# Performance work log

Measured on AMD Instinct MI355X. Metric: run time of the kernel, lower is better.

Reference implementation:

```python
import jax, jax.numpy as jnp
import numpy as np

B, N = 8, 2048          # clouds x points per cloud
M1, M2 = 1024, 256      # centroids after ratio 0.5, then 0.25
K = 64                  # max_num_neighbors
R1, R2 = 0.2, 0.4       # radii
CURV_K = 10             # knn for curvature
CURV_SCALAR = 10.0      # Net(curvature_scalar)
NEG = -1e30


def _sqdist(a, b):
    # squared pairwise distances [len(a), len(b)] without an [.,.,3] intermediate
    return jnp.sum(a * a, -1)[:, None] + jnp.sum(b * b, -1)[None, :] - 2.0 * (a @ b.T)


def _mlp3(x, Wa, ba, Wb, bb, Wc, bc):
    # torch_geometric MLP: Linear+ReLU hidden layers, plain last layer
    h = jax.nn.relu(x @ Wa + ba)
    h = jax.nn.relu(h @ Wb + bb)
    return h @ Wc + bc


def _curvature(pos):
    # per-point surface variation lambda_min / sum(lambda) over k-NN covariance
    d2 = _sqdist(pos, pos)                        # [N,N]
    _, idx = jax.lax.top_k(-d2, CURV_K)           # k nearest (incl. self)
    nbr = pos[idx]                                # [N,k,3]
    c = nbr - jnp.mean(nbr, 1, keepdims=True)
    cov = jnp.einsum('nki,nkj->nij', c, c) / CURV_K
    ev = jnp.linalg.eigvalsh(cov)                 # ascending
    return ev[:, 0] / (jnp.sum(ev, -1) + 1e-8)


def _fps_weighted(pos, curv, m):
    # farthest point sampling, min-distance score weighted by curvature
    w = 1.0 + CURV_SCALAR * curv
    d0 = jnp.sum((pos - pos[0]) ** 2, -1)
    def step(min_d2, _):
        i = jnp.argmax(min_d2 * w)
        nd = jnp.sum((pos - pos[i]) ** 2, -1)
        return jnp.minimum(min_d2, nd), i
    _, rest = jax.lax.scan(step, d0, None, length=m - 1)
    return jnp.concatenate([jnp.zeros((1,), rest.dtype), rest])


def _sa(x, pos, curv, m, r, params):
    # SAModule: weighted FPS -> radius grouping (cap K) -> PointNetConv (gather, MLP, max)
    idx = _fps_weighted(pos, curv, m)
    cpos = pos[idx]                               # [m,3]
    d2 = _sqdist(cpos, pos)                       # [m,N]
    score = jnp.where(d2 <= r * r, -d2, NEG)
    vals, nidx = jax.lax.top_k(score, K)          # up to K nearest within radius
    mask = vals > NEG * 0.5                       # [m,K]
    rel = pos[nidx] - cpos[:, None, :]            # [m,K,3]
    feats = rel if x is None else jnp.concatenate([x[nidx], rel], -1)
    msg = _mlp3(feats, *params)                   # [m,K,F]
    msg = jnp.where(mask[:, :, None], msg, NEG)
    out = jnp.max(msg, 1)                         # scatter-max aggregation
    out = jnp.where(jnp.any(mask, 1)[:, None], out, 0.0)  # empty groups -> 0
    return out, cpos, curv[idx]


def _forward(pos, W1a, b1a, W1b, b1b, W1c, b1c, W2a, b2a, W2b, b2b, W2c, b2c,
             W3a, b3a, W3b, b3b, W3c, b3c, Wh1, bh1, Wh2, bh2, Wh3, bh3):
    p1 = (W1a, b1a, W1b, b1b, W1c, b1c)
    p2 = (W2a, b2a, W2b, b2b, W2c, b2c)
    p3 = (W3a, b3a, W3b, b3b, W3c, b3c)
    def cloud(p):
        curv = _curvature(p)
        x1, pos1, c1 = _sa(None, p, curv, M1, R1, p1)
        x2, pos2, _ = _sa(x1, pos1, c1, M2, R2, p2)
        g = _mlp3(jnp.concatenate([x2, pos2], -1), *p3)   # [M2,1024]
        return jnp.max(g, 0)                              # global max pool
    gfeat = jax.vmap(cloud)(pos.reshape(B, N, 3))          # [B,1024]
    logits = _mlp3(gfeat, Wh1, bh1, Wh2, bh2, Wh3, bh3)    # dropout (eval) = id
    return jax.nn.log_softmax(logits, -1)


_LAYERS = [("W1a", "b1a", 3, 64), ("W1b", "b1b", 64, 64), ("W1c", "b1c", 64, 128),
           ("W2a", "b2a", 131, 128), ("W2b", "b2b", 128, 128), ("W2c", "b2c", 128, 256),
           ("W3a", "b3a", 259, 256), ("W3b", "b3b", 256, 512), ("W3c", "b3c", 512, 1024),
           ("Wh1", "bh1", 1024, 512), ("Wh2", "bh2", 512, 256), ("Wh3", "bh3", 256, 10)]


def setup_inputs() -> dict:
    key = jax.random.key(0)
    ks = iter(jax.random.split(key, 2 * len(_LAYERS) + 1))
    inp = {"pos": jax.random.uniform(next(ks), (B * N, 3), jnp.float32)}
    for wn, bn, fi, fo in _LAYERS:
        inp[wn] = jax.random.normal(next(ks), (fi, fo), jnp.float32) / np.sqrt(fi)
        inp[bn] = jnp.zeros((fo,), jnp.float32)
    return inp


def reference(pos, W1a, b1a, W1b, b1b, W1c, b1c, W2a, b2a, W2b, b2b, W2c, b2c,
              W3a, b3a, W3b, b3b, W3c, b3c, Wh1, bh1, Wh2, bh2, Wh3, bh3):
    return _forward(pos, W1a, b1a, W1b, b1b, W1c, b1c, W2a, b2a, W2b, b2b, W2c, b2c,
                    W3a, b3a, W3b, b3b, W3c, b3c, Wh1, bh1, Wh2, bh2, Wh3, bh3)
```

## Files before the change

### kernel.cpp

```cpp
#include <hip/hip_runtime.h>
#include <hip/hip_fp16.h>
#include <math.h>

#define TID threadIdx.x

typedef _Float16 h2vec __attribute__((ext_vector_type(2)));
typedef _Float16 f16x8 __attribute__((ext_vector_type(8)));
typedef float f32x4 __attribute__((ext_vector_type(4)));
typedef float f32x2v __attribute__((ext_vector_type(2)));

#if __has_builtin(__builtin_elementwise_fma)
#define EFMA(a, b, c) __builtin_elementwise_fma((a), (b), (c))
#else
static __device__ __forceinline__ f32x2v EFMA(f32x2v a, f32x2v b, f32x2v c) {
    f32x2v r;
    r.x = fmaf(a.x, b.x, c.x);
    r.y = fmaf(a.y, b.y, c.y);
    return r;
}
#endif

static __device__ __forceinline__ float fdot2(unsigned a, unsigned b, float c) {
    h2vec av, bv;
    __builtin_memcpy(&av, &a, 4);
    __builtin_memcpy(&bv, &b, 4);
    return __builtin_amdgcn_fdot2(av, bv, c, false);
}

static __device__ __forceinline__ unsigned packh2(float a, float b) {
    __half2 hh = __floats2half2_rn(a, b);
    unsigned u;
    __builtin_memcpy(&u, &hh, 4);
    return u;
}

static __device__ __forceinline__ unsigned encf(float f) {
    unsigned u = __float_as_uint(f);
    return (u >> 31) ? ~u : (u | 0x80000000u);
}
static __device__ __forceinline__ float decf(unsigned e) {
    unsigned u = (e >> 31) ? (e & 0x7fffffffu) : ~e;
    return __uint_as_float(u);
}

static __device__ __forceinline__ int wave_sum(int v) {
    v += __builtin_amdgcn_update_dpp(0, v, 0x111, 0xf, 0xf, true);
    v += __builtin_amdgcn_update_dpp(0, v, 0x112, 0xf, 0xf, true);
    v += __builtin_amdgcn_update_dpp(0, v, 0x114, 0xf, 0xf, true);
    v += __builtin_amdgcn_update_dpp(0, v, 0x118, 0xf, 0xf, true);
    v += __builtin_amdgcn_update_dpp(0, v, 0x142, 0xf, 0xf, true);
    v += __builtin_amdgcn_update_dpp(0, v, 0x143, 0xf, 0xf, true);
    return __builtin_amdgcn_readlane(v, 63);
}

template <int CTRL>
static __device__ __forceinline__ unsigned long long dpp_max_u64(unsigned long long k) {
    int lo = (int)(unsigned)(k & 0xffffffffULL);
    int hi = (int)(unsigned)(k >> 32);
    int lo2 = __builtin_amdgcn_update_dpp(0, lo, CTRL, 0xf, 0xf, true);
    int hi2 = __builtin_amdgcn_update_dpp(0, hi, CTRL, 0xf, 0xf, true);
    unsigned long long k2 = ((unsigned long long)(unsigned)hi2 << 32) | (unsigned)lo2;
    return k2 > k ? k2 : k;
}

static __device__ __forceinline__ void pack_slot(const float* __restrict__ W,
                                                 unsigned* __restrict__ out,
                                                 int K, int ncols, int t) {
    int lane = t & 63;
    int frag = t >> 6;
    int nct = ncols >> 4;
    int ks = frag / nct, ct = frag - ks * nct;
    int kbase = (ks << 5) + ((lane >> 4) << 3);
    int cc = (ct << 4) + (lane & 15);
    unsigned o[4];
#pragma unroll
    for (int i = 0; i < 4; ++i) {
        int k0 = kbase + 2 * i, k1 = kbase + 2 * i + 1;
        float f0 = (k0 < K) ? W[(size_t)k0 * ncols + cc] : 0.f;
        float f1 = (k1 < K) ? W[(size_t)k1 * ncols + cc] : 0.f;
        o[i] = packh2(f0, f1);
    }
    *(uint4*)&out[(size_t)t * 4] = make_uint4(o[0], o[1], o[2], o[3]);
}

__global__ __launch_bounds__(256) void curv_kernel(const float* __restrict__ pos,
                                                   float* __restrict__ curv) {
    __shared__ float4 sp[2048];
    __shared__ float smd[64][40];
    __shared__ int smi[64][40];
    int cloud = blockIdx.x >> 5;
    int base = cloud << 11;
    for (int j = TID; j < 2048; j += 256) {
        const float* p = pos + (size_t)(base + j) * 3;
        float x = p[0], y = p[1], z = p[2];
        sp[j] = make_float4(x, y, z, fmaf(x, x, fmaf(y, y, z * z)));
    }
    __syncthreads();
    int pt = TID >> 2;
    int sub = TID & 3;
    int li = ((blockIdx.x & 31) << 6) + pt;
    float4 pi = sp[li];
    float bd[10];
    int bi[10];
#pragma unroll
    for (int t = 0; t < 10; ++t) { bd[t] = 3.0e38f; bi[t] = 0; }
    int j0 = sub << 9;
    for (int jj = 0; jj < 512; ++jj) {
        int j = j0 + jj;
        float4 pj = sp[j];
        float dot = fmaf(pi.x, pj.x, fmaf(pi.y, pj.y, pi.z * pj.z));
        float d2 = pi.w + pj.w - 2.0f * dot;
        if (d2 < bd[9]) {
            bd[9] = d2; bi[9] = j;
#pragma unroll
            for (int t = 9; t > 0; --t) {
                if (bd[t] < bd[t - 1]) {
                    float td = bd[t]; bd[t] = bd[t - 1]; bd[t - 1] = td;
                    int ti = bi[t]; bi[t] = bi[t - 1]; bi[t - 1] = ti;
                }
            }
        }
    }
#pragma unroll
    for (int t = 0; t < 10; ++t) {
        smd[pt][sub * 10 + t] = bd[t];
        smi[pt][sub * 10 + t] = bi[t];
    }
    __syncthreads();
    float d0 = smd[pt][0], d1 = smd[pt][10], d2h = smd[pt][20], d3 = smd[pt][30];
    int i0 = smi[pt][0], i1 = smi[pt][10], i2 = smi[pt][20], i3 = smi[pt][30];
    int h0 = 0, h1 = 0, h2c = 0, h3 = 0;
    int mbi[10];
#pragma unroll
    for (int t = 0; t < 10; ++t) {
        bool a01 = (d1 < d0) || (d1 == d0 && i1 < i0);
        float dA = a01 ? d1 : d0; int iA = a01 ? i1 : i0;
        bool a23 = (d3 < d2h) || (d3 == d2h && i3 < i2);
        float dB = a23 ? d3 : d2h; int iB = a23 ? i3 : i2;
        bool ab = (dB < dA) || (dB == dA && iB < iA);
        mbi[t] = ab ? iB : iA;
        if (ab) {
            if (a23) { ++h3; d3 = (h3 < 10) ? smd[pt][30 + h3] : 3.0e38f;
                       i3 = (h3 < 10) ? smi[pt][30 + h3] : 0x7fffffff; }
            else     { ++h2c; d2h = (h2c < 10) ? smd[pt][20 + h2c] : 3.0e38f;
                       i2 = (h2c < 10) ? smi[pt][20 + h2c] : 0x7fffffff; }
        } else {
            if (a01) { ++h1; d1 = (h1 < 10) ? smd[pt][10 + h1] : 3.0e38f;
                       i1 = (h1 < 10) ? smi[pt][10 + h1] : 0x7fffffff; }
            else     { ++h0; d0 = (h0 < 10) ? smd[pt][h0] : 3.0e38f;
                       i0 = (h0 < 10) ? smi[pt][h0] : 0x7fffffff; }
        }
    }
    if (sub != 0) return;
    double sx = 0, sy = 0, sz = 0;
#pragma unroll
    for (int t = 0; t < 10; ++t) { float4 p = sp[mbi[t]]; sx += p.x; sy += p.y; sz += p.z; }
    double mx = sx / 10.0, my = sy / 10.0, mz = sz / 10.0;
    double cxx = 0, cxy = 0, cxz = 0, cyy = 0, cyz = 0, czz = 0;
#pragma unroll
    for (int t = 0; t < 10; ++t) {
        float4 p = sp[mbi[t]];
        double dx = p.x - mx, dy = p.y - my, dz = p.z - mz;
        cxx += dx * dx; cxy += dx * dy; cxz += dx * dz;
        cyy += dy * dy; cyz += dy * dz; czz += dz * dz;
    }
    cxx /= 10.0; cxy /= 10.0; cxz /= 10.0; cyy /= 10.0; cyz /= 10.0; czz /= 10.0;
    double q = (cxx + cyy + czz) / 3.0;
    double b00 = cxx - q, b11 = cyy - q, b22 = czz - q;
    double p2 = b00 * b00 + b11 * b11 + b22 * b22 +
                2.0 * (cxy * cxy + cxz * cxz + cyz * cyz);
    double lmin;
    if (p2 <= 0.0) {
        lmin = q;
    } else {
        double p = sqrt(p2 / 6.0);
        double inv = 1.0 / p;
        double c00 = b00 * inv, c01 = cxy * inv, c02 = cxz * inv;
        double c11 = b11 * inv, c12 = cyz * inv, c22 = b22 * inv;
        double detB = c00 * (c11 * c22 - c12 * c12)
                    - c01 * (c01 * c22 - c12 * c02)
                    + c02 * (c01 * c12 - c11 * c02);
        double r = 0.5 * detB;
        r = fmin(1.0, fmax(-1.0, r));
        double phi = acos(r) / 3.0;
        lmin = q + 2.0 * p * cos(phi + 2.0943951023931953);
    }
    double s3 = cxx + cyy + czz;
    curv[base + li] = (float)(lmin / (s3 + 1e-8));
}

template <int N, int M, int SLOTS>
static __device__ void fps_body(
    const float* __restrict__ srcpos, int stride, const float* __restrict__ srccurv,
    int cloud, float4* __restrict__ outPos, float* __restrict__ outCurv,
    float* __restrict__ outA, int ldA,
    float4* sp, int* sidx, unsigned long long* rec ) {
    constexpr int PAIRS = SLOTS / 2;
    const float* cp = srcpos + (size_t)cloud * N * stride;
    for (int j = TID; j < N; j += 256)
        sp[j] = make_float4(cp[j * stride], cp[j * stride + 1], cp[j * stride + 2], 0.f);
    if (TID == 0) sidx[0] = 0;
    __syncthreads();
    f32x2v px[PAIRS], py[PAIRS], pz[PAIRS], md[PAIRS], wvv[PAIRS];
#pragma unroll
    for (int s = 0; s < PAIRS; ++s) {
        int p0 = ((2 * s) << 8) + TID, p1 = ((2 * s + 1) << 8) + TID;
        float4 q0 = sp[p0], q1 = sp[p1];
        px[s].x = q0.x; px[s].y = q1.x;
        py[s].x = q0.y; py[s].y = q1.y;
        pz[s].x = q0.z; pz[s].y = q1.z;
        md[s].x = 3.0e38f; md[s].y = 3.0e38f;
        wvv[s].x = fmaf(10.0f, srccurv[cloud * N + p0], 1.0f);
        wvv[s].y = fmaf(10.0f, srccurv[cloud * N + p1], 1.0f);
    }
    int lane = TID & 63, w4 = TID >> 6;
    float4 c0 = sp[0];
    float cx = c0.x, cy = c0.y, cz = c0.z;
    for (int t = 1; t < M; ++t) {
        f32x2v cxv, cyv, czv;
        cxv.x = cx; cxv.y = cx; cyv.x = cy; cyv.y = cy; czv.x = cz; czv.y = cz;
        unsigned long long kk[PAIRS];
#pragma unroll
        for (int s = 0; s < PAIRS; ++s) {
            f32x2v dx = px[s] - cxv, dy = py[s] - cyv, dz = pz[s] - czv;
            f32x2v nd = EFMA(dx, dx, EFMA(dy, dy, dz * dz));
            f32x2v m2 = __builtin_elementwise_min(md[s], nd);
            md[s] = m2;
            f32x2v sc = m2 * wvv[s];
            unsigned long long k0 =
                ((unsigned long long)__float_as_uint(sc.x) << 32) |
                (unsigned)(2047 - (((2 * s) << 8) + TID));
            unsigned long long k1 =
                ((unsigned long long)__float_as_uint(sc.y) << 32) |
                (unsigned)(2047 - (((2 * s + 1) << 8) + TID));
            kk[s] = k0 > k1 ? k0 : k1;
        }
        unsigned long long k = kk[0];
#pragma unroll
        for (int s = 1; s < PAIRS; ++s) k = kk[s] > k ? kk[s] : k;
        k = dpp_max_u64<0x111>(k);
        k = dpp_max_u64<0x112>(k);
        k = dpp_max_u64<0x114>(k);
        k = dpp_max_u64<0x118>(k);
        k = dpp_max_u64<0x142>(k);
        k = dpp_max_u64<0x143>(k);
        int pbase = (t & 1) << 2;
        if (lane == 63) rec[pbase | w4] = k;
        __syncthreads();
        unsigned long long k0 = rec[pbase + 0];
        unsigned long long k1 = rec[pbase + 1];
        unsigned long long k2 = rec[pbase + 2];
        unsigned long long k3 = rec[pbase + 3];
        unsigned long long ka = k0 > k1 ? k0 : k1;
        unsigned long long kb = k2 > k3 ? k2 : k3;
        unsigned long long km = ka > kb ? ka : kb;
        int nbix = 2047 - (int)(unsigned)(km & 0xffffffffULL);
        if (TID == 0) sidx[t] = nbix;
        float4 cc = sp[nbix];
        cx = cc.x; cy = cc.y; cz = cc.z;
    }
    __syncthreads();
    for (int j = TID; j < M; j += 256) {
        int id = sidx[j];
        float4 qv = sp[id];
        outPos[cloud * M + j] = qv;
        if (outCurv) outCurv[cloud * M + j] = srccurv[cloud * N + id];
        if (outA) {
            float* a = outA + (size_t)(cloud * M + j) * ldA;
            a[256] = qv.x; a[257] = qv.y; a[258] = qv.z;
        }
    }
}

__global__ __launch_bounds__(256, 1) void fps1_pack_kernel(
    const float* __restrict__ pos, const float* __restrict__ curv,
    float4* __restrict__ pos1, float* __restrict__ curv1,
    const float* __restrict__ Wc, const float* __restrict__ Wa,
    const float* __restrict__ Wb, const float* __restrict__ W3a,
    const float* __restrict__ W3b, const float* __restrict__ W3c,
    unsigned* __restrict__ WcH, unsigned* __restrict__ WaH,
    unsigned* __restrict__ WbH, unsigned* __restrict__ W3aH,
    unsigned* __restrict__ W3bH, unsigned* __restrict__ W3cH,
    unsigned* __restrict__ gfeatE) {
    __shared__ float4 sp[2048];
    __shared__ int sidx[1024];
    __shared__ unsigned long long rec[8];
    if (blockIdx.x < 8) {
        fps_body<2048, 1024, 8>(pos, 3, curv, blockIdx.x, pos1, curv1, nullptr, 0,
                                sp, sidx, rec);
        return;
    }
    int b = blockIdx.x - 8;
    if (b == 0)
        for (int i = TID; i < 8192; i += 256) gfeatE[i] = 0u;
    if (b < 16)        pack_slot(Wc,  WcH,  128, 256,  b * 256 + TID);
    else if (b < 26)   pack_slot(Wa,  WaH,  131, 128,  (b - 16) * 256 + TID);
    else if (b < 34)   pack_slot(Wb,  WbH,  128, 128,  (b - 26) * 256 + TID);
    else if (b < 70)   pack_slot(W3a, W3aH, 259, 256,  (b - 34) * 256 + TID);
    else if (b < 134)  pack_slot(W3b, W3bH, 256, 512,  (b - 70) * 256 + TID);
    else               pack_slot(W3c, W3cH, 512, 1024, (b - 134) * 256 + TID);
}

template <int NCH>
static __device__ __forceinline__ int select_k64_reg(
    const unsigned* __restrict__ ck, const int* __restrict__ ci,
    int c, int lane, int* sel, int* nbOut) {
    if (c <= 64) {
        *nbOut = c;
        return (lane < c) ? ci[lane] : 0;
    }
    unsigned long long kq[NCH];
    bool act[NCH];
#pragma unroll
    for (int q = 0; q < NCH; ++q) {
        int idx = (q << 6) + lane;
        bool v = idx < c;
        act[q] = v;
        kq[q] = v ? (((unsigned long long)ck[idx] << 32) | (unsigned)ci[idx]) : 0ULL;
    }
    int excess = c - 64;
    if (excess <= 24) {
        for (int r = 0; r < excess; ++r) {
            unsigned long long k = 0;
#pragma unroll
            for (int q = 0; q < NCH; ++q) {
                unsigned long long kc = act[q] ? kq[q] : 0ULL;
                k = kc > k ? kc : k;
            }
            k = dpp_max_u64<0x111>(k);
            k = dpp_max_u64<0x112>(k);
            k = dpp_max_u64<0x114>(k);
            k = dpp_max_u64<0x118>(k);
            k = dpp_max_u64<0x142>(k);
            k = dpp_max_u64<0x143>(k);
            unsigned klo = (unsigned)__builtin_amdgcn_readlane(
                (int)(unsigned)(k & 0xffffffffULL), 63);
            unsigned khi = (unsigned)__builtin_amdgcn_readlane(
                (int)(unsigned)(k >> 32), 63);
            unsigned long long km = ((unsigned long long)khi << 32) | klo;
#pragma unroll
            for (int q = 0; q < NCH; ++q)
                if (act[q] && kq[q] == km) act[q] = false;
        }
    } else {
        unsigned T = 0;
        for (int bit = 31; bit >= 0; --bit) {
            unsigned mid = T | (1u << bit);
            int cl = 0;
#pragma unroll
            for (int q = 0; q < NCH; ++q)
                cl += (act[q] && (unsigned)(kq[q] >> 32) < mid) ? 1 : 0;
            if (wave_sum(cl) < 64) T = mid;
        }
        int cl = 0;
#pragma unroll
        for (int q = 0; q < NCH; ++q)
            cl += (act[q] && (unsigned)(kq[q] >> 32) < T) ? 1 : 0;
        int need = 64 - wave_sum(cl);
        int TI = 0;
        for (int bit = 11; bit >= 0; --bit) {
            int mid = TI | (1 << bit);
            int ce = 0;
#pragma unroll
            for (int q = 0; q < NCH; ++q)
                ce += (act[q] && (unsigned)(kq[q] >> 32) == T &&
                       (int)(unsigned)(kq[q] & 0xffffffffULL) < mid) ? 1 : 0;
            if (wave_sum(ce) < need) TI = mid;
        }
#pragma unroll
        for (int q = 0; q < NCH; ++q) {
            unsigned hi = (unsigned)(kq[q] >> 32);
            int lo = (int)(unsigned)(kq[q] & 0xffffffffULL);
            act[q] = act[q] && (hi < T || (hi == T && lo <= TI));
        }
    }
    int base = 0;
#pragma unroll
    for (int q = 0; q < NCH; ++q) {
        unsigned long long m = __ballot(act[q]);
        if (act[q]) {
            int off = __popcll(m & ((1ULL << lane) - 1));
            sel[base + off] = (int)(unsigned)(kq[q] & 0xffffffffULL);
        }
        base += __popcll(m);
    }
    *nbOut = 64;
    return sel[lane];
}

union U1 {
    struct {
        float4 sp[2048];
        unsigned ck[4][256];
        int ci[4][256];
        int sel[4][64];
    } p;
    unsigned h2s[4][2048];
};

static __device__ void conv1_body(
    int bid, U1& u,
    const float* __restrict__ pos, const float4* __restrict__ pos1,
    const float* __restrict__ W1, const float* __restrict__ B1,
    const float* __restrict__ W2, const float* __restrict__ B2,
    const float* __restrict__ W3, const float* __restrict__ B3,
    float* __restrict__ x1) {
    __shared__ int nbs[4];
    int cloud = bid >> 8;
    int w4 = TID >> 6, lane = TID & 63;
    int centb = (bid & 255) << 2;
    int g = (cloud << 10) + centb + w4;
    int base = cloud << 11;
    for (int j = TID; j < 2048; j += 256) {
        const float* p = pos + (size_t)(base + j) * 3;
        u.p.sp[j] = make_float4(p[0], p[1], p[2], 0.f);
    }
    __syncthreads();
    float4 cq = pos1[g];
    double cx = cq.x, cy = cq.y, cz = cq.z;
    int cnt = 0;
    for (int s = 0; s < 32; ++s) {
        int j = (s << 6) + lane;
        float4 pj = u.p.sp[j];
        double dx = (double)pj.x - cx, dy = (double)pj.y - cy, dz = (double)pj.z - cz;
        double d2 = dx * dx + dy * dy + dz * dz;
        bool in = (d2 <= 0.2 * 0.2);
        unsigned long long m = __ballot(in);
        if (in) {
            int p = cnt + __popcll(m & ((1ULL << lane) - 1));
            if (p < 256) {
                u.p.ck[w4][p] = __float_as_uint((float)d2);
                u.p.ci[w4][p] = j;
            }
        }
        cnt += __popcll(m);
    }
    int c = min(cnt, 256);
    int nb;
    int idxn = select_k64_reg<4>(u.p.ck[w4], u.p.ci[w4], c, lane, u.p.sel[w4], &nb);
    if (lane == 0) nbs[w4] = nb;
    float4 pn = u.p.sp[idxn];
    float rx = pn.x - cq.x, ry = pn.y - cq.y, rz = pn.z - cq.z;
    __syncthreads();
    float h1[64];
#pragma unroll
    for (int cc2 = 0; cc2 < 64; ++cc2) {
        float v = fmaf(rx, W1[cc2], fmaf(ry, W1[64 + cc2], fmaf(rz, W1[128 + cc2], B1[cc2])));
        h1[cc2] = fmaxf(v, 0.f);
    }
#pragma unroll 1
    for (int half = 0; half < 2; ++half) {
        int c0 = half << 5;
        float h2[32];
#pragma unroll
        for (int t = 0; t < 32; ++t) h2[t] = B2[c0 + t];
#pragma unroll
        for (int i = 0; i < 64; ++i) {
            float hv = h1[i];
            const float* wr = W2 + i * 64 + c0;
#pragma unroll
            for (int t = 0; t < 32; ++t) h2[t] = fmaf(hv, wr[t], h2[t]);
        }
#pragma unroll
        for (int t = 0; t < 32; ++t) h2[t] = fmaxf(h2[t], 0.f);
        unsigned* hrow = &u.h2s[w4][lane << 5];
        int sw = (lane & 7) << 2;
#pragma unroll
        for (int q = 0; q < 4; ++q) {
            unsigned tmp[4];
#pragma unroll
            for (int k2 = 0; k2 < 4; ++k2) {
                int jp = (q << 2) + k2;
                tmp[k2] = packh2(h2[2 * jp], h2[2 * jp + 1]);
            }
            int qg = (half << 2) + q;
            *(uint4*)&hrow[(qg << 2) ^ sw] = make_uint4(tmp[0], tmp[1], tmp[2], tmp[3]);
        }
    }
    __syncthreads();
    int ch = ((w4 & 1) << 6) + lane;
    int cbase = (w4 >> 1) << 1;
    unsigned w2[32];
#pragma unroll
    for (int p = 0; p < 32; ++p)
        w2[p] = packh2(W3[(2 * p) * 128 + ch], W3[(2 * p + 1) * 128 + ch]);
    float bv = B3[ch];
#pragma unroll 1
    for (int ci2 = 0; ci2 < 2; ++ci2) {
        int cc = cbase + ci2;
        int nbc = nbs[cc];
        float m = -1e30f;
        for (int n = 0; n < nbc; ++n) {
            const unsigned* hr = &u.h2s[cc][n << 5];
            int sw2 = (n & 7) << 2;
            float a0 = 0.f, a1 = 0.f, a2 = 0.f, a3 = 0.f;
#pragma unroll
            for (int q = 0; q < 8; ++q) {
                uint4 hv = *(const uint4*)&hr[(q << 2) ^ sw2];
                a0 = fdot2(hv.x, w2[(q << 2) + 0], a0);
                a1 = fdot2(hv.y, w2[(q << 2) + 1], a1);
                a2 = fdot2(hv.z, w2[(q << 2) + 2], a2);
                a3 = fdot2(hv.w, w2[(q << 2) + 3], a3);
            }
            m = fmaxf(m, bv + (a0 + a1) + (a2 + a3));
        }
        x1[(size_t)((cloud << 10) + centb + cc) * 128 + ch] = m;
    }
}

union UM {
    U1 c;
    struct {
        float4 sp[1024];
        unsigned long long rec[8];
        int sidx[256];
    } f;
};

__global__ __launch_bounds__(256, 3) void fps2_conv1_kernel(
    const float* __restrict__ pos, const float4* __restrict__ pos1,
    const float* __restrict__ curv1, float4* __restrict__ pos2,
    float* __restrict__ Abuf,
    const float* __restrict__ W1, const float* __restrict__ B1,
    const float* __restrict__ W2, const float* __restrict__ B2,
    const float* __restrict__ W3, const float* __restrict__ B3,
    float* __restrict__ x1) {
    __shared__ UM u;
    if (blockIdx.x < 8) {
        fps_body<1024, 256, 4>((const float*)pos1, 4, curv1, blockIdx.x, pos2,
                               nullptr, Abuf, 260, u.f.sp, u.f.sidx, u.f.rec);
    } else {
        conv1_body(blockIdx.x - 8, u.c, pos, pos1, W1, B1, W2, B2, W3, B3, x1);
    }
}

union U2 {
    struct {
        float4 sp[1024];
        unsigned ck[4][512];
        int ci[4][512];
        int sel[4][64];
    } p;
    unsigned xs[4][5376];
};

__global__ __launch_bounds__(256, 1) void conv2_kernel(
    const float4* __restrict__ pos1, const float4* __restrict__ pos2,
    const float* __restrict__ x1,
    const unsigned* __restrict__ WaH, const float* __restrict__ Ba,
    const unsigned* __restrict__ WbH, const float* __restrict__ Bb,
    const unsigned* __restrict__ WcH, const float* __restrict__ Bc,
    float* __restrict__ Aout) {
    __shared__ U2 u;
    __shared__ unsigned h1s[4][4352];
    __shared__ int nbs[4];
    int cloud = blockIdx.x >> 6;
    int w4 = TID >> 6, lane = TID & 63;
    int centb = (blockIdx.x & 63) << 2;
    int g = (cloud << 8) + centb + w4;
    int quad = lane >> 4, l15 = lane & 15;
    for (int j = TID; j < 1024; j += 256) u.p.sp[j] = pos1[(cloud << 10) + j];
    __syncthreads();
    float4 cq = pos2[g];
    double cx = cq.x, cy = cq.y, cz = cq.z;
    int cnt = 0;
    for (int s = 0; s < 16; ++s) {
        int j = (s << 6) + lane;
        float4 pj = u.p.sp[j];
        double dx = (double)pj.x - cx, dy = (double)pj.y - cy, dz = (double)pj.z - cz;
        double d2 = dx * dx + dy * dy + dz * dz;
        bool in = (d2 <= 0.4 * 0.4);
        unsigned long long m = __ballot(in);
        if (in) {
            int p = cnt + __popcll(m & ((1ULL << lane) - 1));
            if (p < 512) {
                u.p.ck[w4][p] = __float_as_uint((float)d2);
                u.p.ci[w4][p] = j;
            }
        }
        cnt += __popcll(m);
    }
    int c = min(cnt, 512);
    int nb;
    int idxn = select_k64_reg<8>(u.p.ck[w4], u.p.ci[w4], c, lane, u.p.sel[w4], &nb);
    if (lane == 0) nbs[w4] = nb;
    float4 pn = u.p.sp[idxn];
    float rx = pn.x - cq.x, ry = pn.y - cq.y, rz = pn.z - cq.z;
    __syncthreads();
    {
        const float4* xr = (const float4*)(x1 + (size_t)((cloud << 10) + idxn) * 128);
        unsigned* row = &u.xs[w4][lane * 84];
#pragma unroll
        for (int q = 0; q < 16; ++q) {
            float4 a = xr[q * 2], b = xr[q * 2 + 1];
            *(uint4*)&row[q << 2] = make_uint4(packh2(a.x, a.y), packh2(a.z, a.w),
                                               packh2(b.x, b.y), packh2(b.z, b.w));
        }
        *(uint4*)&row[64] = make_uint4(packh2(rx, ry), packh2(rz, 0.f), 0u, 0u);
        *(uint4*)&row[68] = make_uint4(0u, 0u, 0u, 0u);
        *(uint4*)&row[72] = make_uint4(0u, 0u, 0u, 0u);
        *(uint4*)&row[76] = make_uint4(0u, 0u, 0u, 0u);
    }
    float ba8[8];
#pragma unroll
    for (int ct = 0; ct < 8; ++ct) ba8[ct] = Ba[(ct << 4) + l15];
#pragma unroll 1
    for (int ct = 0; ct < 8; ++ct) {
        f16x8 bfrag[5];
#pragma unroll
        for (int ks = 0; ks < 5; ++ks) {
            uint4 bv = *(const uint4*)&WaH[(size_t)((((ks << 3) | ct) << 6) | lane) << 2];
            __builtin_memcpy(&bfrag[ks], &bv, 16);
        }
#pragma unroll
        for (int rt = 0; rt < 4; ++rt) {
            f32x4 acc = {0.f, 0.f, 0.f, 0.f};
#pragma unroll
            for (int ks = 0; ks < 5; ++ks) {
                f16x8 af;
                uint4 av = *(const uint4*)&u.xs[w4][((rt << 4) + l15) * 84 +
                                                    (((ks << 2) + quad) << 2)];
                __builtin_memcpy(&af, &av, 16);
                acc = __builtin_amdgcn_mfma_f32_16x16x32_f16(af, bfrag[ks], acc, 0, 0, 0);
            }
#pragma unroll
            for (int r = 0; r < 4; ++r) {
                float v = fmaxf(acc[r] + ba8[ct], 0.f);
                float vp = __shfl_xor(v, 1, 64);
                if (!(l15 & 1)) {
                    int rowi = (rt << 4) + (quad << 2) + r;
                    h1s[w4][rowi * 68 + (ct << 3) + (l15 >> 1)] = packh2(v, vp);
                }
            }
        }
    }
    unsigned* h2w = &u.xs[w4][0];
#pragma unroll
    for (int ct = 0; ct < 8; ++ct) ba8[ct] = Bb[(ct << 4) + l15];
#pragma unroll 1
    for (int ct = 0; ct < 8; ++ct) {
        f16x8 bfrag[4];
#pragma unroll
        for (int ks = 0; ks < 4; ++ks) {
            uint4 bv = *(const uint4*)&WbH[(size_t)((((ks << 3) | ct) << 6) | lane) << 2];
            __builtin_memcpy(&bfrag[ks], &bv, 16);
        }
#pragma unroll
        for (int rt = 0; rt < 4; ++rt) {
            f32x4 acc = {0.f, 0.f, 0.f, 0.f};
#pragma unroll
            for (int ks = 0; ks < 4; ++ks) {
                f16x8 af;
                uint4 av = *(const uint4*)&h1s[w4][((rt << 4) + l15) * 68 +
                                                   (((ks << 2) + quad) << 2)];
                __builtin_memcpy(&af, &av, 16);
                acc = __builtin_amdgcn_mfma_f32_16x16x32_f16(af, bfrag[ks], acc, 0, 0, 0);
            }
#pragma unroll
            for (int r = 0; r < 4; ++r) {
                float v = fmaxf(acc[r] + ba8[ct], 0.f);
                float vp = __shfl_xor(v, 1, 64);
                if (!(l15 & 1)) {
                    int rowi = (rt << 4) + (quad << 2) + r;
                    int d = (ct << 3) + (l15 >> 1);
                    int ch = d >> 2, din = d & 3;
                    h2w[(rowi << 6) + ((ch ^ (rowi & 15)) << 2) + din] = packh2(v, vp);
                }
            }
        }
    }
    __syncthreads();
    int ctb = w4 << 2;
    f16x8 cfrag[4][4];
#pragma unroll
    for (int ct = 0; ct < 4; ++ct)
#pragma unroll
        for (int ks = 0; ks < 4; ++ks) {
            uint4 bv = *(const uint4*)&WcH[(size_t)((((ks << 4) | (ctb + ct)) << 6) | lane) << 2];
            __builtin_memcpy(&cfrag[ct][ks], &bv, 16);
        }
#pragma unroll 1
    for (int cent = 0; cent < 4; ++cent) {
        const unsigned* h2r = &u.xs[cent][0];
        int nbc = nbs[cent];
        float runM[4][4];
#pragma unroll
        for (int ct = 0; ct < 4; ++ct)
#pragma unroll
            for (int r = 0; r < 4; ++r) runM[ct][r] = -1e30f;
#pragma unroll
        for (int rt = 0; rt < 4; ++rt) {
            int nl = (rt << 4) + l15;
            f16x8 afrag[4];
#pragma unroll
            for (int ks = 0; ks < 4; ++ks) {
                int cp = ((ks << 2) | quad) ^ l15;
                uint4 av = *(const uint4*)&h2r[(nl << 6) + (cp << 2)];
                __builtin_memcpy(&afrag[ks], &av, 16);
            }
#pragma unroll
            for (int ct = 0; ct < 4; ++ct) {
                f32x4 acc = {0.f, 0.f, 0.f, 0.f};
#pragma unroll
                for (int ks = 0; ks < 4; ++ks)
                    acc = __builtin_amdgcn_mfma_f32_16x16x32_f16(afrag[ks], cfrag[ct][ks],
                                                                 acc, 0, 0, 0);
                int nb0 = (rt << 4) + (quad << 2);
#pragma unroll
                for (int r = 0; r < 4; ++r) {
                    float v = (nb0 + r < nbc) ? acc[r] : -1e30f;
                    runM[ct][r] = fmaxf(runM[ct][r], v);
                }
            }
        }
#pragma unroll
        for (int ct = 0; ct < 4; ++ct) {
            float m = fmaxf(fmaxf(runM[ct][0], runM[ct][1]),
                            fmaxf(runM[ct][2], runM[ct][3]));
            m = fmaxf(m, __shfl_xor(m, 16, 64));
            m = fmaxf(m, __shfl_xor(m, 32, 64));
            if (lane < 16) {
                int cc = ((ctb + ct) << 4) | l15;
                Aout[(size_t)((cloud << 8) + centb + cent) * 260 + cc] = m + Bc[cc];
            }
        }
    }
}

__global__ __launch_bounds__(256) void gemm_mfma2(
    const float* __restrict__ A, int lda, const unsigned* __restrict__ Bp, int nct,
    const float* __restrict__ bias, float* __restrict__ C, int ldc, int K,
    int relu, unsigned* __restrict__ gmax) {
    int w = (blockIdx.x << 2) + (TID >> 6);
    int ncg = nct >> 3;
    int rs = w / ncg, cg = w - rs * ncg;
    int r0 = rs << 4, ct0 = cg << 3;
    int lane = TID & 63, quad = lane >> 4, l15 = lane & 15;
    f32x4 acc[8];
#pragma unroll
    for (int ct = 0; ct < 8; ++ct) acc[ct] = (f32x4){0.f, 0.f, 0.f, 0.f};
    const float* ar = A + (size_t)(r0 + l15) * lda;
    int nks = (K + 31) >> 5;
    for (int ks = 0; ks < nks; ++ks) {
        int kb = (ks << 5) + (quad << 3);
        f16x8 af;
        if (kb + 8 <= K) {
            float4 a0 = *(const float4*)(ar + kb);
            float4 a1 = *(const float4*)(ar + kb + 4);
            uint4 av = make_uint4(packh2(a0.x, a0.y), packh2(a0.z, a0.w),
                                  packh2(a1.x, a1.y), packh2(a1.z, a1.w));
            __builtin_memcpy(&af, &av, 16);
        } else {
            float f[8];
#pragma unroll
            for (int j = 0; j < 8; ++j) f[j] = (kb + j < K) ? ar[kb + j] : 0.f;
            uint4 av = make_uint4(packh2(f[0], f[1]), packh2(f[2], f[3]),
                                  packh2(f[4], f[5]), packh2(f[6], f[7]));
            __builtin_memcpy(&af, &av, 16);
        }
#pragma unroll
        for (int ct = 0; ct < 8; ++ct) {
            uint4 bv = *(const uint4*)&Bp[(size_t)(((ks * nct + ct0 + ct) << 6) | lane) << 2];
            f16x8 bf;
            __builtin_memcpy(&bf, &bv, 16);
            acc[ct] = __builtin_amdgcn_mfma_f32_16x16x32_f16(af, bf, acc[ct], 0, 0, 0);
        }
    }
    if (!gmax) {
#pragma unroll
        for (int ct = 0; ct < 8; ++ct) {
            int col = ((ct0 + ct) << 4) + l15;
            float bb = bias[col];
#pragma unroll
            for (int r = 0; r < 4; ++r) {
                int row = r0 + (quad << 2) + r;
                float v = acc[ct][r] + bb;
                if (relu) v = fmaxf(v, 0.f);
                C[(size_t)row * ldc + col] = v;
            }
        }
    } else {
        int cloud = r0 >> 8;
#pragma unroll
        for (int ct = 0; ct < 8; ++ct) {
            int col = ((ct0 + ct) << 4) + l15;
            float bb = bias[col];
            float m = fmaxf(fmaxf(acc[ct][0], acc[ct][1]),
                            fmaxf(acc[ct][2], acc[ct][3])) + bb;
            m = fmaxf(m, __shfl_xor(m, 16, 64));
            m = fmaxf(m, __shfl_xor(m, 32, 64));
            if (quad == 0) atomicMax(&gmax[(cloud << 10) + col], encf(m));
        }
    }
}

__global__ __launch_bounds__(128) void head1_kernel(
    const unsigned* __restrict__ gfeatE,
    const float* __restrict__ Wh1, const float* __restrict__ bh1,
    float* __restrict__ s1g) {
    int cloud = TID >> 4;
    int col = (blockIdx.x << 4) + (TID & 15);
    float v = bh1[col];
    const unsigned* ge = gfeatE + (cloud << 10);
    for (int i = 0; i < 1024; ++i)
        v = fmaf(decf(ge[i]), Wh1[i * 512 + col], v);
    s1g[(cloud << 9) + col] = fmaxf(v, 0.f);
}

__global__ __launch_bounds__(128) void head2_kernel(
    const float* __restrict__ s1g,
    const float* __restrict__ Wh2, const float* __restrict__ bh2,
    float* __restrict__ s2g) {
    int cloud = TID >> 4;
    int col = (blockIdx.x << 4) + (TID & 15);
    float v = bh2[col];
    const float* s1 = s1g + (cloud << 9);
    for (int i = 0; i < 512; ++i)
        v = fmaf(s1[i], Wh2[i * 256 + col], v);
    s2g[(cloud << 8) + col] = fmaxf(v, 0.f);
}

__global__ __launch_bounds__(64) void head3_kernel(
    const float* __restrict__ s2g,
    const float* __restrict__ Wh3, const float* __restrict__ bh3,
    float* __restrict__ out) {
    __shared__ float lg[10];
    int cloud = blockIdx.x;
    const float* s2 = s2g + (cloud << 8);
    if (TID < 10) {
        float v = bh3[TID];
        for (int i = 0; i < 256; ++i) v = fmaf(s2[i], Wh3[i * 10 + TID], v);
        lg[TID] = v;
    }
    __syncthreads();
    if (TID == 0) {
        float mx = lg[0];
        for (int i = 1; i < 10; ++i) mx = fmaxf(mx, lg[i]);
        float s = 0.f;
        for (int i = 0; i < 10; ++i) s += expf(lg[i] - mx);
        float lse = mx + logf(s);
        for (int i = 0; i < 10; ++i) out[cloud * 10 + i] = lg[i] - lse;
    }
}

extern "C" void kernel_launch(void* const* d_in, const int* in_sizes, int n_in,
                              void* d_out, int out_size, void* d_ws, size_t ws_size,
                              hipStream_t stream) {
    (void)in_sizes; (void)n_in; (void)out_size; (void)ws_size;
    const float* pos = (const float*)d_in[0];
    const float* W1a = (const float*)d_in[1];  const float* b1a = (const float*)d_in[2];
    const float* W1b = (const float*)d_in[3];  const float* b1b = (const float*)d_in[4];
    const float* W1c = (const float*)d_in[5];  const float* b1c = (const float*)d_in[6];
    const float* W2a = (const float*)d_in[7];  const float* b2a = (const float*)d_in[8];
    const float* W2b = (const float*)d_in[9];  const float* b2b = (const float*)d_in[10];
    const float* W2c = (const float*)d_in[11]; const float* b2c = (const float*)d_in[12];
    const float* W3a = (const float*)d_in[13]; const float* b3a = (const float*)d_in[14];
    const float* W3b = (const float*)d_in[15]; const float* b3b = (const float*)d_in[16];
    const float* W3c = (const float*)d_in[17]; const float* b3c = (const float*)d_in[18];
    const float* Wh1 = (const float*)d_in[19]; const float* bh1 = (const float*)d_in[20];
    const float* Wh2 = (const float*)d_in[21]; const float* bh2 = (const float*)d_in[22];
    const float* Wh3 = (const float*)d_in[23]; const float* bh3 = (const float*)d_in[24];

    char* ws = (char*)d_ws;
    float*    curv   = (float*)(ws + 0);
    float4*   pos1   = (float4*)(ws + 98304);
    float*    curv1  = (float*)(ws + 229376);
    float4*   pos2   = (float4*)(ws + 270336);
    unsigned* gfeatE = (unsigned*)(ws + 303104);
    unsigned* WcH    = (unsigned*)(ws + 335872);
    unsigned* WaH    = (unsigned*)(ws + 401408);
    unsigned* WbH    = (unsigned*)(ws + 442368);
    float*    x1     = (float*)(ws + 524288);
    float*    Abuf   = (float*)(ws + 4718592);
    float*    h1g    = (float*)(ws + 6848512);
    unsigned* W3aH   = (unsigned*)(ws + 8945664);
    unsigned* W3bH   = (unsigned*)(ws + 9093120);
    unsigned* W3cH   = (unsigned*)(ws + 9355264);
    float*    h2g    = x1;
    float*    s1g    = h1g;
    float*    s2g    = h1g + 4096;

    curv_kernel<<<256, 256, 0, stream>>>(pos, curv);
    fps1_pack_kernel<<<398, 256, 0, stream>>>(pos, curv, pos1, curv1,
                                              W2c, W2a, W2b, W3a, W3b, W3c,
                                              WcH, WaH, WbH, W3aH, W3bH, W3cH,
                                              gfeatE);
    fps2_conv1_kernel<<<2056, 256, 0, stream>>>(pos, pos1, curv1, pos2, Abuf,
                                                W1a, b1a, W1b, b1b, W1c, b1c, x1);
    conv2_kernel<<<512, 256, 0, stream>>>(pos1, pos2, x1, WaH, b2a, WbH, b2b, WcH, b2c,
                                          Abuf);
    gemm_mfma2<<<64, 256, 0, stream>>>(Abuf, 260, W3aH, 16, b3a, h1g, 256,
                                       259, 1, nullptr);
    gemm_mfma2<<<128, 256, 0, stream>>>(h1g, 256, W3bH, 32, b3b, h2g, 512,
                                        256, 1, nullptr);
    gemm_mfma2<<<256, 256, 0, stream>>>(h2g, 512, W3cH, 64, b3c, nullptr, 0,
                                        512, 0, gfeatE);
    head1_kernel<<<32, 128, 0, stream>>>(gfeatE, Wh1, bh1, s1g);
    head2_kernel<<<16, 128, 0, stream>>>(s1g, Wh2, bh2, s2g);
    head3_kernel<<<8, 64, 0, stream>>>(s2g, Wh3, bh3, (float*)d_out);
}
```

Measured before the change: 1.170 ms.

## Move conv1 second and third MLP layers onto fp16 MFMA with prepacked weights

The scalar FMA loop for conv1's 64x64 layer and the dot2-based 64x128 layer become MFMA 16x16x32 f16 tiles. Hidden activations are staged in padded LDS rows, and the max over neighbours is taken from the accumulator fragments using cross-lane shuffles. W1b and W1c are now packed into fragment layout by extra blocks in the earlier pack kernel. This removes per-thread scalar FMA work, at the cost of extra block syncs and fp16 rounding of the first hidden layer.

```diff
diff --git a/kernel.cpp b/kernel.cpp
--- a/kernel.cpp
+++ b/kernel.cpp
@@ -278,9 +278,11 @@
     const float* __restrict__ Wc, const float* __restrict__ Wa,
     const float* __restrict__ Wb, const float* __restrict__ W3a,
     const float* __restrict__ W3b, const float* __restrict__ W3c,
+    const float* __restrict__ W1b, const float* __restrict__ W1c,
     unsigned* __restrict__ WcH, unsigned* __restrict__ WaH,
     unsigned* __restrict__ WbH, unsigned* __restrict__ W3aH,
     unsigned* __restrict__ W3bH, unsigned* __restrict__ W3cH,
+    unsigned* __restrict__ W1bH, unsigned* __restrict__ W1cH,
     unsigned* __restrict__ gfeatE) {
     __shared__ float4 sp[2048];
     __shared__ int sidx[1024];
@@ -298,7 +300,9 @@
     else if (b < 34)   pack_slot(Wb,  WbH,  128, 128,  (b - 26) * 256 + TID);
     else if (b < 70)   pack_slot(W3a, W3aH, 259, 256,  (b - 34) * 256 + TID);
     else if (b < 134)  pack_slot(W3b, W3bH, 256, 512,  (b - 70) * 256 + TID);
-    else               pack_slot(W3c, W3cH, 512, 1024, (b - 134) * 256 + TID);
+    else if (b < 390)  pack_slot(W3c, W3cH, 512, 1024, (b - 134) * 256 + TID);
+    else if (b < 392)  pack_slot(W1b, W1bH, 64, 64,    (b - 390) * 256 + TID);
+    else               pack_slot(W1c, W1cH, 64, 128,   (b - 392) * 256 + TID);
 }
 
 template <int NCH>
@@ -395,19 +399,20 @@
         int ci[4][256];
         int sel[4][64];
     } p;
-    unsigned h2s[4][2048];
+    unsigned hs[4][2304];
 };
 
 static __device__ void conv1_body(
     int bid, U1& u,
     const float* __restrict__ pos, const float4* __restrict__ pos1,
     const float* __restrict__ W1, const float* __restrict__ B1,
-    const float* __restrict__ W2, const float* __restrict__ B2,
-    const float* __restrict__ W3, const float* __restrict__ B3,
+    const unsigned* __restrict__ W1bH, const float* __restrict__ B2,
+    const unsigned* __restrict__ W1cH, const float* __restrict__ B3,
     float* __restrict__ x1) {
     __shared__ int nbs[4];
     int cloud = bid >> 8;
     int w4 = TID >> 6, lane = TID & 63;
+    int quad = lane >> 4, l15 = lane & 15;
     int centb = (bid & 255) << 2;
     int g = (cloud << 10) + centb + w4;
     int base = cloud << 11;
@@ -441,70 +446,124 @@
     if (lane == 0) nbs[w4] = nb;
     float4 pn = u.p.sp[idxn];
     float rx = pn.x - cq.x, ry = pn.y - cq.y, rz = pn.z - cq.z;
-    __syncthreads();
     float h1[64];
 #pragma unroll
     for (int cc2 = 0; cc2 < 64; ++cc2) {
         float v = fmaf(rx, W1[cc2], fmaf(ry, W1[64 + cc2], fmaf(rz, W1[128 + cc2], B1[cc2])));
         h1[cc2] = fmaxf(v, 0.f);
     }
+    __syncthreads();
+    {
+        unsigned* row = &u.hs[w4][lane * 36];
+#pragma unroll
+        for (int q = 0; q < 8; ++q) {
+            *(uint4*)&row[q << 2] =
+                make_uint4(packh2(h1[8 * q + 0], h1[8 * q + 1]),
+                           packh2(h1[8 * q + 2], h1[8 * q + 3]),
+                           packh2(h1[8 * q + 4], h1[8 * q + 5]),
+                           packh2(h1[8 * q + 6], h1[8 * q + 7]));
+        }
+    }
+    __syncthreads();
+    {
+        f16x8 bfrag[2][4];
+#pragma unroll
+        for (int ks = 0; ks < 2; ++ks)
+#pragma unroll
+            for (int ct = 0; ct < 4; ++ct) {
+                uint4 bv = *(const uint4*)&W1bH[(size_t)(
+                    (((ks << 2) | ct) << 6) | lane) << 2];
+                __builtin_memcpy(&bfrag[ks][ct], &bv, 16);
+            }
+        f16x8 af[4][2];
+#pragma unroll
+        for (int rt = 0; rt < 4; ++rt)
+#pragma unroll
+            for (int ks = 0; ks < 2; ++ks) {
+                uint4 av = *(const uint4*)&u.hs[w4][((rt << 4) + l15) * 36 +
+                                                    (((ks << 2) | quad) << 2)];
+                __builtin_memcpy(&af[rt][ks], &av, 16);
+            }
+        float ba4[4];
+#pragma unroll
+        for (int ct = 0; ct < 4; ++ct) ba4[ct] = B2[(ct << 4) + l15];
+#pragma unroll
+        for (int rt = 0; rt < 4; ++rt) {
+#pragma unroll
+            for (int ct = 0; ct < 4; ++ct) {
+                f32x4 acc = {0.f, 0.f, 0.f, 0.f};
+#pragma unroll
+                for (int ks = 0; ks < 2; ++ks)
+                    acc = __builtin_amdgcn_mfma_f32_16x16x32_f16(
+                        af[rt][ks], bfrag[ks][ct], acc, 0, 0, 0);
+#pragma unroll
+                for (int r = 0; r < 4; ++r) {
+                    float v = fmaxf(acc[r] + ba4[ct], 0.f);
+                    float vp = __shfl_xor(v, 1, 64);
+                    if (!(l15 & 1)) {
+                        int rowi = (rt << 4) + (quad << 2) + r;
+                        u.hs[w4][rowi * 36 + (ct << 3) + (l15 >> 1)] = packh2(v, vp);
+                    }
+                }
+            }
+        }
+    }
+    __syncthreads();
+    {
+        int ct2 = w4 << 1;
+        f16x8 cfrag[2][2];
+#pragma unroll
+        for (int ctl = 0; ctl < 2; ++ctl)
+#pragma unroll
+            for (int ks = 0; ks < 2; ++ks) {
+                uint4 bv = *(const uint4*)&W1cH[(size_t)(
+                    (((ks << 3) | (ct2 + ctl)) << 6) | lane) << 2];
+                __builtin_memcpy(&cfrag[ctl][ks], &bv, 16);
+            }
 #pragma unroll 1
-    for (int half = 0; half < 2; ++half) {
-        int c0 = half << 5;
-        float h2[32];
-#pragma unroll
-        for (int t = 0; t < 32; ++t) h2[t] = B2[c0 + t];
-#pragma unroll
-        for (int i = 0; i < 64; ++i) {
-            float hv = h1[i];
-            const float* wr = W2 + i * 64 + c0;
-#pragma unroll
-            for (int t = 0; t < 32; ++t) h2[t] = fmaf(hv, wr[t], h2[t]);
-        }
-#pragma unroll
-        for (int t = 0; t < 32; ++t) h2[t] = fmaxf(h2[t], 0.f);
-        unsigned* hrow = &u.h2s[w4][lane << 5];
-        int sw = (lane & 7) << 2;
-#pragma unroll
-        for (int q = 0; q < 4; ++q) {
-            unsigned tmp[4];
-#pragma unroll
-            for (int k2 = 0; k2 < 4; ++k2) {
-                int jp = (q << 2) + k2;
-                tmp[k2] = packh2(h2[2 * jp], h2[2 * jp + 1]);
-            }
-            int qg = (half << 2) + q;
-            *(uint4*)&hrow[(qg << 2) ^ sw] = make_uint4(tmp[0], tmp[1], tmp[2], tmp[3]);
-        }
-    }
-    __syncthreads();
-    int ch = ((w4 & 1) << 6) + lane;
-    int cbase = (w4 >> 1) << 1;
-    unsigned w2[32];
-#pragma unroll
-    for (int p = 0; p < 32; ++p)
-        w2[p] = packh2(W3[(2 * p) * 128 + ch], W3[(2 * p + 1) * 128 + ch]);
-    float bv = B3[ch];
-#pragma unroll 1
-    for (int ci2 = 0; ci2 < 2; ++ci2) {
-        int cc = cbase + ci2;
-        int nbc = nbs[cc];
-        float m = -1e30f;
-        for (int n = 0; n < nbc; ++n) {
-            const unsigned* hr = &u.h2s[cc][n << 5];
-            int sw2 = (n & 7) << 2;
-            float a0 = 0.f, a1 = 0.f, a2 = 0.f, a3 = 0.f;
-#pragma unroll
-            for (int q = 0; q < 8; ++q) {
-                uint4 hv = *(const uint4*)&hr[(q << 2) ^ sw2];
-                a0 = fdot2(hv.x, w2[(q << 2) + 0], a0);
-                a1 = fdot2(hv.y, w2[(q << 2) + 1], a1);
-                a2 = fdot2(hv.z, w2[(q << 2) + 2], a2);
-                a3 = fdot2(hv.w, w2[(q << 2) + 3], a3);
-            }
-            m = fmaxf(m, bv + (a0 + a1) + (a2 + a3));
-        }
-        x1[(size_t)((cloud << 10) + centb + cc) * 128 + ch] = m;
+        for (int cent = 0; cent < 4; ++cent) {
+            int nbc = nbs[cent];
+            float runM[2][4];
+#pragma unroll
+            for (int ctl = 0; ctl < 2; ++ctl)
+#pragma unroll
+                for (int r = 0; r < 4; ++r) runM[ctl][r] = -1e30f;
+#pragma unroll
+            for (int rt = 0; rt < 4; ++rt) {
+                f16x8 af[2];
+#pragma unroll
+                for (int ks = 0; ks < 2; ++ks) {
+                    uint4 av = *(const uint4*)&u.hs[cent][((rt << 4) + l15) * 36 +
+                                                          (((ks << 2) | quad) << 2)];
+                    __builtin_memcpy(&af[ks], &av, 16);
+                }
+#pragma unroll
+                for (int ctl = 0; ctl < 2; ++ctl) {
+                    f32x4 acc = {0.f, 0.f, 0.f, 0.f};
+#pragma unroll
+                    for (int ks = 0; ks < 2; ++ks)
+                        acc = __builtin_amdgcn_mfma_f32_16x16x32_f16(
+                            af[ks], cfrag[ctl][ks], acc, 0, 0, 0);
+                    int nb0 = (rt << 4) + (quad << 2);
+#pragma unroll
+                    for (int r = 0; r < 4; ++r) {
+                        float v = (nb0 + r < nbc) ? acc[r] : -1e30f;
+                        runM[ctl][r] = fmaxf(runM[ctl][r], v);
+                    }
+                }
+            }
+#pragma unroll
+            for (int ctl = 0; ctl < 2; ++ctl) {
+                float m = fmaxf(fmaxf(runM[ctl][0], runM[ctl][1]),
+                                fmaxf(runM[ctl][2], runM[ctl][3]));
+                m = fmaxf(m, __shfl_xor(m, 16, 64));
+                m = fmaxf(m, __shfl_xor(m, 32, 64));
+                if (lane < 16) {
+                    int cc = ((ct2 + ctl) << 4) | l15;
+                    x1[(size_t)((cloud << 10) + centb + cent) * 128 + cc] = m + B3[cc];
+                }
+            }
+        }
     }
 }
 
@@ -522,15 +581,15 @@
     const float* __restrict__ curv1, float4* __restrict__ pos2,
     float* __restrict__ Abuf,
     const float* __restrict__ W1, const float* __restrict__ B1,
-    const float* __restrict__ W2, const float* __restrict__ B2,
-    const float* __restrict__ W3, const float* __restrict__ B3,
+    const unsigned* __restrict__ W1bH, const float* __restrict__ B2,
+    const unsigned* __restrict__ W1cH, const float* __restrict__ B3,
     float* __restrict__ x1) {
     __shared__ UM u;
     if (blockIdx.x < 8) {
         fps_body<1024, 256, 4>((const float*)pos1, 4, curv1, blockIdx.x, pos2,
                                nullptr, Abuf, 260, u.f.sp, u.f.sidx, u.f.rec);
     } else {
-        conv1_body(blockIdx.x - 8, u.c, pos, pos1, W1, B1, W2, B2, W3, B3, x1);
+        conv1_body(blockIdx.x - 8, u.c, pos, pos1, W1, B1, W1bH, B2, W1cH, B3, x1);
     }
 }
 
@@ -870,6 +929,8 @@
     unsigned* WcH    = (unsigned*)(ws + 335872);
     unsigned* WaH    = (unsigned*)(ws + 401408);
     unsigned* WbH    = (unsigned*)(ws + 442368);
+    unsigned* W1bH   = (unsigned*)(ws + 475136);
+    unsigned* W1cH   = (unsigned*)(ws + 483328);
     float*    x1     = (float*)(ws + 524288);
     float*    Abuf   = (float*)(ws + 4718592);
     float*    h1g    = (float*)(ws + 6848512);
@@ -881,12 +942,14 @@
     float*    s2g    = h1g + 4096;
 
     curv_kernel<<<256, 256, 0, stream>>>(pos, curv);
-    fps1_pack_kernel<<<398, 256, 0, stream>>>(pos, curv, pos1, curv1,
+    fps1_pack_kernel<<<404, 256, 0, stream>>>(pos, curv, pos1, curv1,
                                               W2c, W2a, W2b, W3a, W3b, W3c,
+                                              W1b, W1c,
                                               WcH, WaH, WbH, W3aH, W3bH, W3cH,
+                                              W1bH, W1cH,
                                               gfeatE);
     fps2_conv1_kernel<<<2056, 256, 0, stream>>>(pos, pos1, curv1, pos2, Abuf,
-                                                W1a, b1a, W1b, b1b, W1c, b1c, x1);
+                                                W1a, b1a, W1bH, b1b, W1cH, b1c, x1);
     conv2_kernel<<<512, 256, 0, stream>>>(pos1, pos2, x1, WaH, b2a, WbH, b2b, WcH, b2c,
                                           Abuf);
     gemm_mfma2<<<64, 256, 0, stream>>>(Abuf, 260, W3aH, 16, b3a, h1g, 256,
```

Result: faster. 1.068 ms (-8.7%).
